# Performance work log

Measured on AMD Instinct MI355X. Metric: run time of the kernel, lower is better.

The kernel has to match this reference:

```python
import jax, jax.numpy as jnp
import numpy as np

B, N, IN, OUT, H = 16, 1024, 512, 512, 4

def setup_inputs() -> dict:
    key = jax.random.key(0)
    ks = jax.random.split(key, 10)
    s = 0.03  # small init scale to keep tanh/sigmoid in sane range
    return {
        "h": jax.random.normal(ks[0], (B, N, IN), jnp.float32),
        "adj": jax.random.randint(ks[1], (B, N, N), 0, 2) > 0,
        "W": jax.random.normal(ks[2], (H, OUT, IN), jnp.float32) * s,   # per-head Linear weight [out,in]
        "bW": jax.random.normal(ks[3], (H, OUT), jnp.float32) * s,
        "attn": jax.random.normal(ks[4], (H, OUT, OUT), jnp.float32) * s,
        "A_w": jax.random.normal(ks[5], (OUT, OUT * H), jnp.float32) * s,
        "fc_w": jax.random.normal(ks[6], (OUT, IN), jnp.float32) * s,
        "g1_w": jax.random.normal(ks[7], (OUT, OUT), jnp.float32) * s,
        "g2_w": jax.random.normal(ks[8], (OUT, OUT), jnp.float32) * s,
        "gbias": jax.random.normal(ks[9], (OUT,), jnp.float32) * s,
    }

def reference(h, adj, W, bW, attn, A_w, fc_w, g1_w, g2_w, gbias):
    # Per-head projection: Wh[b,h,n,o] = h @ W_h^T + b_h  (dropout is identity at inference)
    Wh = jnp.einsum('bni,hoi->bhno', h, W) + bW[None, :, None, :]
    # Bilinear attention scores: Wh @ attn_h @ Wh^T, masked by adjacency, then tanh
    e = jnp.einsum('bhno,hop->bhnp', Wh, attn)          # [B,H,N,O]
    scores = jnp.einsum('bhnp,bhmp->bhnm', e, Wh)       # [B,H,N,N]
    A_mat = jnp.tanh(jnp.where(adj[:, None, :, :], scores, 0.0))
    # Aggregate neighbors and relu
    hp = jax.nn.relu(jnp.einsum('bhnm,bhmo->bhno', A_mat, Wh))  # [B,H,N,O]
    # Concat heads (relu of relu is identity), project with A
    cat = jnp.transpose(hp, (0, 2, 1, 3)).reshape(hp.shape[0], hp.shape[2], -1)  # [B,N,H*O]
    ha = cat @ A_w.T                                     # [B,N,O]
    hf = h @ fc_w.T                                      # [B,N,O]
    # Sigmoid-gated fusion of the two branches
    coeff = jax.nn.sigmoid(hf @ g1_w.T + ha @ g2_w.T + gbias)
    return hf * coeff + ha * (1.0 - coeff)
```

## Files before the change

### kernel.cpp

```cpp
#include <hip/hip_runtime.h>
#include <hip/hip_fp16.h>


typedef _Float16 h8 __attribute__((ext_vector_type(8)));
typedef _Float16 h4 __attribute__((ext_vector_type(4)));
typedef float f4 __attribute__((ext_vector_type(4)));

__device__ __forceinline__ void load_lds16(const void* g, void* l) {
  __builtin_amdgcn_global_load_lds(
      (const __attribute__((address_space(1))) unsigned int*)g,
      (__attribute__((address_space(3))) unsigned int*)l, 16, 0, 0);
}

struct GP {
  const _Float16* A; const _Float16* B; void* C; const float* bias;
  const unsigned long long* adjb; _Float16* aux;
  int K, ldA, ldB, ldC, z0, ntx, nty, nz;
  long sAz, sAb, sBz, sBh, sCz, sCb, sCh, sBiasH, sAuxZ;
};

__device__ __forceinline__ void stage_chunk(const _Float16* G, long ld, int koff,
                                            _Float16* S, int c, int rs, int cs) {
  int r = c * 8 + rs;
  int kb = (cs ^ (r & 7)) * 8;
  load_lds16(G + (long)r * ld + koff + kb, S + c * 512);
}

template<int EPI>
__device__ __forceinline__ void gemm_pipe(GP p, char* smem) {
  const int tid = threadIdx.x;
  const int wv = tid >> 6;
  const int ln = tid & 63;
  const int l15 = ln & 15;
  const int lg = ln >> 4;
  const int wr = wv >> 2, wc = wv & 3;
  const int rs = ln >> 3;
  const int cs = ln & 7;

  const int bid = blockIdx.x;
  const int ntile = p.ntx * p.nty;
  int zl, tx, ty;
  if (p.nz > 1) {
    int xcd = bid & 7;
    int u = bid >> 3;
    zl = xcd + 8 * (u / ntile);
    int t = u % ntile;
    tx = t % p.ntx;
    ty = t / p.ntx;
  } else {
    int xcd = bid & 7;
    int u = bid >> 3;
    int t = xcd * (ntile >> 3) + u;
    zl = 0;
    tx = t % p.ntx;
    ty = t / p.ntx;
  }
  const int zg = p.z0 + zl;
  const int bg = zg >> 2, hg = zg & 3;
  const _Float16* A = p.A + p.sAz * zl + p.sAb * bg;
  const _Float16* Bm = p.B + p.sBz * zl + p.sBh * hg;
  const long m0 = (long)tx * 128;
  const long n0 = (long)ty * 256;
  const int nk = p.K >> 6;

  const _Float16* Ag = A + m0 * p.ldA;
  const _Float16* Bg = Bm + n0 * p.ldB;

  f4 acc[4][4];
#pragma unroll
  for (int i = 0; i < 4; ++i)
#pragma unroll
    for (int j = 0; j < 4; ++j) acc[i][j] = (f4)(0.0f);

#define ABUF(i) ((_Float16*)(smem + (i) * 49152))
#define BBUF(i) ((_Float16*)(smem + (i) * 49152 + 16384))

#pragma unroll
  for (int t0 = 0; t0 < 2; ++t0) {
    if (t0 < nk) {
      _Float16* As = ABUF(t0);
      _Float16* Bs = BBUF(t0);
      const int ko = t0 * 64;
      stage_chunk(Bg, p.ldB, ko, Bs, wv * 2, rs, cs);
      stage_chunk(Bg, p.ldB, ko, Bs, wv * 2 + 1, rs, cs);
      stage_chunk(Bg, p.ldB, ko, Bs, 16 + wv * 2, rs, cs);
      stage_chunk(Bg, p.ldB, ko, Bs, 16 + wv * 2 + 1, rs, cs);
      stage_chunk(Ag, p.ldA, ko, As, wv * 2, rs, cs);
      stage_chunk(Ag, p.ldA, ko, As, wv * 2 + 1, rs, cs);
    }
  }
  if (nk > 1) asm volatile("s_waitcnt vmcnt(6)" ::: "memory");
  else        asm volatile("s_waitcnt vmcnt(0)" ::: "memory");
  __builtin_amdgcn_sched_barrier(0);
  __builtin_amdgcn_s_barrier();

  for (int t = 0; t < nk; ++t) {
    _Float16* As = ABUF(t % 3);
    _Float16* Bs = BBUF(t % 3);
    const int t2 = t + 2;
    const bool st = (t2 < nk);
    _Float16* As2 = ABUF(t2 % 3);
    _Float16* Bs2 = BBUF(t2 % 3);
    const int ko2 = t2 * 64;
#pragma unroll
    for (int ph = 0; ph < 4; ++ph) {
      if (st) {
        if (ph == 0) {
          stage_chunk(Bg, p.ldB, ko2, Bs2, wv * 2, rs, cs);
          stage_chunk(Bg, p.ldB, ko2, Bs2, wv * 2 + 1, rs, cs);
        } else if (ph == 1) {
          stage_chunk(Bg, p.ldB, ko2, Bs2, 16 + wv * 2, rs, cs);
          stage_chunk(Bg, p.ldB, ko2, Bs2, 16 + wv * 2 + 1, rs, cs);
        } else if (ph == 2) {
          stage_chunk(Ag, p.ldA, ko2, As2, wv * 2, rs, cs);
          stage_chunk(Ag, p.ldA, ko2, As2, wv * 2 + 1, rs, cs);
        }
      }
      const int ks = ph >> 1, mp = ph & 1;
      const int kby = ks * 64 + lg * 16;
      h8 av[2], bv[4];
#pragma unroll
      for (int m2 = 0; m2 < 2; ++m2) {
        int row = wr * 64 + (mp * 2 + m2) * 16 + l15;
        av[m2] = *(const h8*)((const char*)As + row * 128 + (kby ^ ((row & 7) << 4)));
      }
#pragma unroll
      for (int n = 0; n < 4; ++n) {
        int col = wc * 64 + n * 16 + l15;
        bv[n] = *(const h8*)((const char*)Bs + col * 128 + (kby ^ ((col & 7) << 4)));
      }
      __builtin_amdgcn_s_barrier();
      __builtin_amdgcn_s_setprio(1);
#pragma unroll
      for (int m2 = 0; m2 < 2; ++m2)
#pragma unroll
        for (int n = 0; n < 4; ++n)
          acc[mp * 2 + m2][n] =
              __builtin_amdgcn_mfma_f32_16x16x32_f16(av[m2], bv[n], acc[mp * 2 + m2][n], 0, 0, 0);
      __builtin_amdgcn_s_setprio(0);
    }
    if (t + 1 < nk) {
      if (t + 2 < nk) asm volatile("s_waitcnt vmcnt(6)" ::: "memory");
      else            asm volatile("s_waitcnt vmcnt(0)" ::: "memory");
      __builtin_amdgcn_sched_barrier(0);
      __builtin_amdgcn_s_barrier();
    }
  }

  asm volatile("s_waitcnt vmcnt(0)" ::: "memory");
  __syncthreads();

  _Float16* Cld = (_Float16*)smem;
  const long coff = p.sCz * zl + p.sCb * bg + p.sCh * hg;
  const float* bias = p.bias ? (p.bias + p.sBiasH * hg) : nullptr;
  _Float16* C = (_Float16*)p.C;
  _Float16* X = (EPI == 6) ? (p.aux + p.sAuxZ * zl) : nullptr;
#pragma unroll
  for (int hh = 0; hh < 2; ++hh) {
    if (wr == hh) {
#pragma unroll
      for (int m = 0; m < 4; ++m) {
#pragma unroll
        for (int j = 0; j < 4; ++j) {
          int lrow = m * 16 + lg * 4 + j;
          long grow = m0 + hh * 64 + lrow;
          int vx = (lrow & 3) << 4;
          unsigned long long w;
          if (EPI == 2)
            w = p.adjb[(long)bg * 16384 + grow * 16 + (n0 >> 6) + wc];
#pragma unroll
          for (int n = 0; n < 4; ++n) {
            int lcol = wv * 0 + wc * 64 + n * 16 + l15;
            float v = acc[m][n][j];
            if (EPI == 6) v += bias[n0 + lcol];
            if (EPI == 2) {
              if ((w >> (n * 16 + l15)) & 1ull) {
                float ex = __expf(2.0f * v);
                v = 1.0f - 2.0f * __builtin_amdgcn_rcpf(ex + 1.0f);
              } else v = 0.0f;
            }
            if (EPI == 3) v = v > 0.0f ? v : 0.0f;
            Cld[lrow * 256 + (lcol ^ vx)] = (_Float16)v;
          }
        }
      }
    }
    __syncthreads();
#pragma unroll
    for (int it = 0; it < 4; ++it) {
      int row = it * 16 + (tid >> 5);
      int col0 = (tid & 31) * 8;
      int vx = (row & 3) << 4;
      h8 o = *(const h8*)&Cld[row * 256 + (col0 ^ vx)];
      *(h8*)&C[coff + (m0 + hh * 64 + row) * p.ldC + n0 + col0] = o;
    }
    if (EPI == 6) {
#pragma unroll
      for (int it = 0; it < 4; ++it) {
        int idx = it * 512 + tid;
        int ol = idx >> 3;
        int ml = (idx & 7) * 8;
        h8 o;
#pragma unroll
        for (int j = 0; j < 8; ++j) {
          int mm = ml + j;
          o[j] = Cld[mm * 256 + (ol ^ ((mm & 3) << 4))];
        }
        *(h8*)&X[(n0 + ol) * 1024 + m0 + hh * 64 + ml] = o;
      }
    }
    __syncthreads();
  }
#undef ABUF
#undef BBUF
}

#define GEMM_PIPE_WRAP(name, epi)                                      \
  __global__ __launch_bounds__(512) void name(GP p) {                  \
    extern __shared__ char smem[];                                     \
    gemm_pipe<epi>(p, smem);                                           \
  }
GEMM_PIPE_WRAP(gemm_wh, 6)
GEMM_PIPE_WRAP(gemm_e, 0)
GEMM_PIPE_WRAP(gemm_amat, 2)
GEMM_PIPE_WRAP(gemm_cat, 3)

__device__ __forceinline__ void stage_tiles5(const _Float16* Ag, const _Float16* Bg,
                                             _Float16* As, _Float16* Bs,
                                             int ldA, int ldB, int wv, int rs, int cs) {
#pragma unroll
  for (int ps = 0; ps < 10; ++ps) {
    int c = ps * 4 + wv;
    if (c < 8) {
      int r = c * 8 + rs;
      int kb = (cs ^ (r & 7)) * 8;
      load_lds16(Ag + (long)r * ldA + kb, As + c * 512);
    } else {
      int cb = c - 8;
      int r = cb * 8 + rs;
      int kb = (cs ^ (r & 7)) * 8;
      load_lds16(Bg + (long)r * ldB + kb, Bs + cb * 512);
    }
  }
}

__device__ __forceinline__ void compute_tile5(const _Float16* As, const _Float16* Bs,
                                              f4 acc[4][4], int wv, int l15, int lg) {
#pragma unroll
  for (int ks = 0; ks < 2; ++ks) {
    const int kby = ks * 64 + lg * 16;
    h8 av[4], bv[4];
#pragma unroll
    for (int m = 0; m < 4; ++m) {
      int row = m * 16 + l15;
      av[m] = *(const h8*)((const char*)As + row * 128 + (kby ^ ((row & 7) << 4)));
    }
#pragma unroll
    for (int n = 0; n < 4; ++n) {
      int col = wv * 64 + n * 16 + l15;
      bv[n] = *(const h8*)((const char*)Bs + col * 128 + (kby ^ ((col & 7) << 4)));
    }
#pragma unroll
    for (int m = 0; m < 4; ++m)
#pragma unroll
      for (int n = 0; n < 4; ++n)
        acc[m][n] = __builtin_amdgcn_mfma_f32_16x16x32_f16(av[m], bv[n], acc[m][n], 0, 0, 0);
  }
}

template<int EPI>
__device__ __forceinline__ void gemm_core_sb(GP p) {
  __shared__ __align__(16) char smem[40960];
  _Float16* Ash = (_Float16*)smem;
  _Float16* Bsh = (_Float16*)(smem + 8192);
  _Float16* Cld = (_Float16*)smem;

  const int tid = threadIdx.x;
  const int wv = tid >> 6;
  const int ln = tid & 63;
  const int l15 = ln & 15;
  const int lg = ln >> 4;
  const int rs = ln >> 3;
  const int cs = ln & 7;

  const int bid = blockIdx.x;
  const int ntile = p.ntx * p.nty;
  int xcd = bid & 7;
  int u = bid >> 3;
  int t = xcd * (ntile >> 3) + u;
  int tx = t % p.ntx;
  int ty = t / p.ntx;
  const int bg = 0, hg = 0;
  const _Float16* A = p.A;
  const _Float16* Bm = p.B;
  const long m0 = (long)tx * 64;
  const long n0 = (long)ty * 256;
  const int nk = p.K >> 6;

  f4 acc[4][4];
#pragma unroll
  for (int i = 0; i < 4; ++i)
#pragma unroll
    for (int j = 0; j < 4; ++j) acc[i][j] = (f4)(0.0f);

  const _Float16* Ag = A + m0 * p.ldA;
  const _Float16* Bg = Bm + n0 * p.ldB;

  for (int kt = 0; kt < nk; ++kt) {
    stage_tiles5(Ag + kt * 64, Bg + kt * 64, Ash, Bsh, p.ldA, p.ldB, wv, rs, cs);
    __syncthreads();
    compute_tile5(Ash, Bsh, acc, wv, l15, lg);
    __syncthreads();
  }

  const long coff = 0;
  const float* bias = p.bias;
  _Float16* C = (_Float16*)p.C;
#pragma unroll
  for (int m = 0; m < 4; ++m) {
#pragma unroll
    for (int j = 0; j < 4; ++j) {
      int lrow = m * 16 + lg * 4 + j;
      int vx = (lrow & 3) << 4;
#pragma unroll
      for (int n = 0; n < 4; ++n) {
        int lcol = wv * 64 + n * 16 + l15;
        float v = acc[m][n][j];
        if (EPI == 5) {
          v += bias[n0 + lcol];
          v = __builtin_amdgcn_rcpf(1.0f + __expf(-v));
        }
        Cld[lrow * 256 + (lcol ^ vx)] = (_Float16)v;
      }
    }
  }
  __syncthreads();
#pragma unroll
  for (int it = 0; it < 8; ++it) {
    int row = it * 8 + (tid >> 5);
    int col0 = (tid & 31) * 8;
    int vx = (row & 3) << 4;
    h8 o = *(const h8*)&Cld[row * 256 + (col0 ^ vx)];
    *(h8*)&C[coff + (m0 + row) * p.ldC + n0 + col0] = o;
  }
  (void)bg; (void)hg;
}

#define GEMM_SB_WRAP(name, epi) \
  __global__ __launch_bounds__(256) void name(GP p) { gemm_core_sb<epi>(p); }
GEMM_SB_WRAP(gemm_hf, 0)
GEMM_SB_WRAP(gemm_ha, 0)
GEMM_SB_WRAP(gemm_gate, 5)

__global__ __launch_bounds__(256) void mix_kernel(const _Float16* gcat,
                                                  const _Float16* coeff, float* out) {
  const int stride = gridDim.x * 256;
  for (int g = blockIdx.x * 256 + threadIdx.x; g < 1048576; g += stride) {
    int r = g >> 6, c8 = (g & 63) << 3;
    h8 hf = *(const h8*)&gcat[(long)r * 1024 + c8];
    h8 ha = *(const h8*)&gcat[(long)r * 1024 + 512 + c8];
    h8 cf = *(const h8*)&coeff[(long)r * 512 + c8];
    float o[8];
#pragma unroll
    for (int j = 0; j < 8; ++j) {
      float c = (float)cf[j];
      o[j] = (float)hf[j] * c + (float)ha[j] * (1.0f - c);
    }
    float* op = &out[(long)r * 512 + c8];
    *(float4*)op = make_float4(o[0], o[1], o[2], o[3]);
    *(float4*)(op + 4) = make_float4(o[4], o[5], o[6], o[7]);
  }
}

__global__ void trans_attn(const float* attn, _Float16* attnT) {
  __shared__ _Float16 tl[64][65];
  const long hh = blockIdx.z;
  const float* I = attn + hh * 262144;
  _Float16* O = attnT + hh * 262144;
  const int r0 = blockIdx.x * 64, c0 = blockIdx.y * 64;
  for (int i = threadIdx.x; i < 4096; i += 256) {
    int r = i >> 6, c = i & 63;
    tl[c][r] = (_Float16)I[(long)(r0 + r) * 512 + c0 + c];
  }
  __syncthreads();
  for (int i = threadIdx.x; i < 4096; i += 256) {
    int c = i >> 6, r = i & 63;
    O[(long)(c0 + c) * 512 + r0 + r] = tl[c][r];
  }
}

__global__ void cvt_f16(const float* in, _Float16* out, int n4) {
  int i = blockIdx.x * 256 + threadIdx.x;
  if (i < n4) {
    float4 v = ((const float4*)in)[i];
    h4 o = {(_Float16)v.x, (_Float16)v.y, (_Float16)v.z, (_Float16)v.w};
    ((h4*)out)[i] = o;
  }
}

__global__ void build_gw(const float* g1, const float* g2, _Float16* gw) {
  int i = blockIdx.x * 256 + threadIdx.x;
  int o = i >> 10, k = i & 1023;
  float v = (k < 512) ? g1[o * 512 + k] : g2[o * 512 + (k - 512)];
  gw[i] = (_Float16)v;
}

__global__ void detect_fmt(const unsigned char* adj, int* flags) {
  __shared__ int sa, sb, sc;
  if (threadIdx.x == 0) { sa = 0; sb = 0; sc = 0; }
  __syncthreads();
  int a = 0, b = 0, c = 0;
  for (int i = threadIdx.x; i < 4096; i += 256) {
    if (adj[i]) {
      if (i & 3) a = 1;
      else c = 1;
      if ((i & 7) == 4) b = 1;
    }
  }
  if (a) sa = 1;
  if (b) sb = 1;
  if (c) sc = 1;
  __syncthreads();
  if (threadIdx.x == 0) {
    int fmt;
    if (sa) fmt = sc ? 1 : 3;
    else fmt = sb ? 0 : 2;
    flags[0] = fmt;
  }
}

__global__ void adj_bits(const void* adj, const int* flags, unsigned long long* adjb) {
  long i = (long)blockIdx.x * 256 + threadIdx.x;
  int fmt = flags[0];
  bool v;
  if (fmt == 1) v = ((const unsigned char*)adj)[i] != 0;
  else if (fmt == 3) v = ((const float*)adj)[i] != 0.0f;
  else if (fmt == 2) v = ((const long long*)adj)[i] != 0;
  else v = ((const int*)adj)[i] != 0;
  unsigned long long m = __ballot(v);
  if ((threadIdx.x & 63) == 0) adjb[i >> 6] = m;
}

extern "C" void kernel_launch(void* const* d_in, const int* in_sizes, int n_in,
                              void* d_out, int out_size, void* d_ws, size_t ws_size,
                              hipStream_t stream) {
  const float* h    = (const float*)d_in[0];
  const void*  adj  = d_in[1];
  const float* W    = (const float*)d_in[2];
  const float* bW   = (const float*)d_in[3];
  const float* attn = (const float*)d_in[4];
  const float* A_w  = (const float*)d_in[5];
  const float* fc_w = (const float*)d_in[6];
  const float* g1   = (const float*)d_in[7];
  const float* g2   = (const float*)d_in[8];
  const float* gbias= (const float*)d_in[9];
  float* out = (float*)d_out;
  char* ws = (char*)d_ws;
  (void)in_sizes; (void)n_in; (void)out_size;

  const int PIPE_LDS = 147456;
  hipFuncSetAttribute((const void*)gemm_wh,   hipFuncAttributeMaxDynamicSharedMemorySize, PIPE_LDS);
  hipFuncSetAttribute((const void*)gemm_e,    hipFuncAttributeMaxDynamicSharedMemorySize, PIPE_LDS);
  hipFuncSetAttribute((const void*)gemm_amat, hipFuncAttributeMaxDynamicSharedMemorySize, PIPE_LDS);
  hipFuncSetAttribute((const void*)gemm_cat,  hipFuncAttributeMaxDynamicSharedMemorySize, PIPE_LDS);

  const size_t MB = 1ull << 20;
  const size_t fixedB = 92 * MB;
  int ZCv = 16;
  if (fixedB + 5ull * 64 * MB <= ws_size) ZCv = 64;
  else if (fixedB + 5ull * 32 * MB <= ws_size) ZCv = 32;
  const int nchunk = 64 / ZCv;

  size_t off = 0;
  auto alloc = [&](size_t sz) { size_t o = off; off += (sz + 255) & ~(size_t)255; return o; };
  const size_t oFlags = alloc(256);
  const size_t oH16   = alloc(16 * MB);
  const size_t oW16   = alloc(2 * MB);
  const size_t oAttnT = alloc(2 * MB);
  const size_t oAw16  = alloc(2 * MB);
  const size_t oFc16  = alloc(512 * 1024);
  const size_t oGw16  = alloc(1 * MB);
  const size_t oAdjb  = alloc(2 * MB);
  const size_t oCat   = alloc(64 * MB);
  const size_t oWhC   = alloc((size_t)ZCv * MB);
  const size_t oEC    = alloc((size_t)ZCv * MB);
  const size_t oWhTC  = alloc((size_t)ZCv * MB);
  const size_t oAmatC = alloc((size_t)ZCv * 2 * MB);
  const size_t oGcat  = oWhC;
  const size_t oCoeff = oAmatC;

  int* flags = (int*)(ws + oFlags);
  _Float16* h16   = (_Float16*)(ws + oH16);
  _Float16* W16   = (_Float16*)(ws + oW16);
  _Float16* attnT = (_Float16*)(ws + oAttnT);
  _Float16* Aw16  = (_Float16*)(ws + oAw16);
  _Float16* fc16  = (_Float16*)(ws + oFc16);
  _Float16* gw16  = (_Float16*)(ws + oGw16);
  unsigned long long* adjb = (unsigned long long*)(ws + oAdjb);
  _Float16* cat   = (_Float16*)(ws + oCat);
  _Float16* WhC   = (_Float16*)(ws + oWhC);
  _Float16* eC    = (_Float16*)(ws + oEC);
  _Float16* WhTC  = (_Float16*)(ws + oWhTC);
  _Float16* AmatC = (_Float16*)(ws + oAmatC);
  _Float16* gcat  = (_Float16*)(ws + oGcat);
  _Float16* coeff = (_Float16*)(ws + oCoeff);

  detect_fmt<<<1, 256, 0, stream>>>((const unsigned char*)adj, flags);
  adj_bits<<<65536, 256, 0, stream>>>(adj, flags, adjb);
  cvt_f16<<<8192, 256, 0, stream>>>(h, h16, 2097152);
  cvt_f16<<<1024, 256, 0, stream>>>(W, W16, 262144);
  cvt_f16<<<1024, 256, 0, stream>>>(A_w, Aw16, 262144);
  cvt_f16<<<256, 256, 0, stream>>>(fc_w, fc16, 65536);
  build_gw<<<2048, 256, 0, stream>>>(g1, g2, gw16);
  trans_attn<<<dim3(8, 8, 4), 256, 0, stream>>>(attn, attnT);

  for (int c = 0; c < nchunk; ++c) {
    const int z0 = c * ZCv;
    GP q;
    q = GP{};
    q.A = h16; q.B = W16; q.C = WhC; q.bias = bW; q.aux = WhTC;
    q.K = 512; q.ldA = 512; q.ldB = 512; q.ldC = 512; q.z0 = z0;
    q.ntx = 8; q.nty = 2; q.nz = ZCv;
    q.sAz = 0; q.sAb = 524288; q.sBz = 0; q.sBh = 262144;
    q.sCz = 524288; q.sCb = 0; q.sCh = 0; q.sBiasH = 512; q.sAuxZ = 524288;
    gemm_wh<<<16 * ZCv, 512, PIPE_LDS, stream>>>(q);
    q = GP{};
    q.A = WhC; q.B = attnT; q.C = eC;
    q.K = 512; q.ldA = 512; q.ldB = 512; q.ldC = 512; q.z0 = z0;
    q.ntx = 8; q.nty = 2; q.nz = ZCv;
    q.sAz = 524288; q.sBh = 262144; q.sCz = 524288;
    gemm_e<<<16 * ZCv, 512, PIPE_LDS, stream>>>(q);
    q = GP{};
    q.A = eC; q.B = WhC; q.C = AmatC; q.adjb = adjb;
    q.K = 512; q.ldA = 512; q.ldB = 512; q.ldC = 1024; q.z0 = z0;
    q.ntx = 8; q.nty = 4; q.nz = ZCv;
    q.sAz = 524288; q.sBz = 524288; q.sCz = 1048576;
    gemm_amat<<<32 * ZCv, 512, PIPE_LDS, stream>>>(q);
    q = GP{};
    q.A = AmatC; q.B = WhTC; q.C = cat;
    q.K = 1024; q.ldA = 1024; q.ldB = 1024; q.ldC = 2048; q.z0 = z0;
    q.sAz = 1048576; q.sBz = 524288;
    q.ntx = 8; q.nty = 2; q.nz = ZCv;
    q.sCz = 0; q.sCb = 2097152; q.sCh = 512;
    gemm_cat<<<16 * ZCv, 512, PIPE_LDS, stream>>>(q);
  }

  GP q;
  q = GP{};
  q.A = h16; q.B = fc16; q.C = gcat;
  q.K = 512; q.ldA = 512; q.ldB = 512; q.ldC = 1024; q.z0 = 0;
  q.ntx = 256; q.nty = 2; q.nz = 1;
  gemm_hf<<<512, 256, 0, stream>>>(q);
  q = GP{};
  q.A = cat; q.B = Aw16; q.C = gcat + 512;
  q.K = 2048; q.ldA = 2048; q.ldB = 2048; q.ldC = 1024; q.z0 = 0;
  q.ntx = 256; q.nty = 2; q.nz = 1;
  gemm_ha<<<512, 256, 0, stream>>>(q);
  q = GP{};
  q.A = gcat; q.B = gw16; q.C = coeff; q.bias = gbias;
  q.K = 1024; q.ldA = 1024; q.ldB = 1024; q.ldC = 512; q.z0 = 0;
  q.ntx = 256; q.nty = 2; q.nz = 1;
  gemm_gate<<<512, 256, 0, stream>>>(q);
  mix_kernel<<<2048, 256, 0, stream>>>(gcat, coeff, out);
}
```

Before: 537.0 us.

## Restructure pipelined GEMM main loop into two half-steps with fewer barriers

Reorganizes the triple-buffered GEMM inner loop. Each k-tile is now split into two halves over N: all A fragments plus half the B fragments are loaded at once, and the next-tile global->LDS staging is interleaved between them. This cuts the per-iteration barrier count from five to two and changes the B staging chunk assignment per wave. It also removes some dead variables in the small GEMM. The cost is more registers held for A fragments, and a different overlap pattern between MFMA work and LDS/global traffic.

```diff
diff --git a/kernel.cpp b/kernel.cpp
--- a/kernel.cpp
+++ b/kernel.cpp
@@ -75,76 +75,83 @@
 #define ABUF(i) ((_Float16*)(smem + (i) * 49152))
 #define BBUF(i) ((_Float16*)(smem + (i) * 49152 + 16384))
 
-#pragma unroll
-  for (int t0 = 0; t0 < 2; ++t0) {
-    if (t0 < nk) {
-      _Float16* As = ABUF(t0);
-      _Float16* Bs = BBUF(t0);
-      const int ko = t0 * 64;
-      stage_chunk(Bg, p.ldB, ko, Bs, wv * 2, rs, cs);
-      stage_chunk(Bg, p.ldB, ko, Bs, wv * 2 + 1, rs, cs);
-      stage_chunk(Bg, p.ldB, ko, Bs, 16 + wv * 2, rs, cs);
-      stage_chunk(Bg, p.ldB, ko, Bs, 16 + wv * 2 + 1, rs, cs);
-      stage_chunk(Ag, p.ldA, ko, As, wv * 2, rs, cs);
-      stage_chunk(Ag, p.ldA, ko, As, wv * 2 + 1, rs, cs);
-    }
-  }
+#define STAGE_A(t)                                                      \
+  { _Float16* As_ = ABUF((t) % 3); const int ko_ = (t) * 64;            \
+    stage_chunk(Ag, p.ldA, ko_, As_, wv * 2, rs, cs);                   \
+    stage_chunk(Ag, p.ldA, ko_, As_, wv * 2 + 1, rs, cs); }
+#define STAGE_B1(t)                                                     \
+  { _Float16* Bs_ = BBUF((t) % 3);                                      \
+    stage_chunk(Bg, p.ldB, (t) * 64, Bs_, wv * 4, rs, cs); }
+#define STAGE_B3(t)                                                     \
+  { _Float16* Bs_ = BBUF((t) % 3); const int ko_ = (t) * 64;            \
+    stage_chunk(Bg, p.ldB, ko_, Bs_, wv * 4 + 1, rs, cs);               \
+    stage_chunk(Bg, p.ldB, ko_, Bs_, wv * 4 + 2, rs, cs);               \
+    stage_chunk(Bg, p.ldB, ko_, Bs_, wv * 4 + 3, rs, cs); }
+
+  STAGE_A(0) STAGE_B1(0) STAGE_B3(0)
+  if (nk > 1) { STAGE_A(1) STAGE_B1(1) STAGE_B3(1) }
   if (nk > 1) asm volatile("s_waitcnt vmcnt(6)" ::: "memory");
   else        asm volatile("s_waitcnt vmcnt(0)" ::: "memory");
   __builtin_amdgcn_sched_barrier(0);
-  __builtin_amdgcn_s_barrier();
+  asm volatile("s_barrier" ::: "memory");
 
   for (int t = 0; t < nk; ++t) {
-    _Float16* As = ABUF(t % 3);
-    _Float16* Bs = BBUF(t % 3);
-    const int t2 = t + 2;
-    const bool st = (t2 < nk);
-    _Float16* As2 = ABUF(t2 % 3);
-    _Float16* Bs2 = BBUF(t2 % 3);
-    const int ko2 = t2 * 64;
-#pragma unroll
-    for (int ph = 0; ph < 4; ++ph) {
-      if (st) {
-        if (ph == 0) {
-          stage_chunk(Bg, p.ldB, ko2, Bs2, wv * 2, rs, cs);
-          stage_chunk(Bg, p.ldB, ko2, Bs2, wv * 2 + 1, rs, cs);
-        } else if (ph == 1) {
-          stage_chunk(Bg, p.ldB, ko2, Bs2, 16 + wv * 2, rs, cs);
-          stage_chunk(Bg, p.ldB, ko2, Bs2, 16 + wv * 2 + 1, rs, cs);
-        } else if (ph == 2) {
-          stage_chunk(Ag, p.ldA, ko2, As2, wv * 2, rs, cs);
-          stage_chunk(Ag, p.ldA, ko2, As2, wv * 2 + 1, rs, cs);
-        }
+    const _Float16* As = ABUF(t % 3);
+    const _Float16* Bs = BBUF(t % 3);
+    const bool st2 = (t + 2 < nk);
+    h8 av[4][2], bv[2][2];
+#pragma unroll
+    for (int m = 0; m < 4; ++m)
+#pragma unroll
+      for (int ks = 0; ks < 2; ++ks) {
+        int row = wr * 64 + m * 16 + l15;
+        int kby = ks * 64 + lg * 16;
+        av[m][ks] = *(const h8*)((const char*)As + row * 128 + (kby ^ ((row & 7) << 4)));
       }
-      const int ks = ph >> 1, mp = ph & 1;
-      const int kby = ks * 64 + lg * 16;
-      h8 av[2], bv[4];
-#pragma unroll
-      for (int m2 = 0; m2 < 2; ++m2) {
-        int row = wr * 64 + (mp * 2 + m2) * 16 + l15;
-        av[m2] = *(const h8*)((const char*)As + row * 128 + (kby ^ ((row & 7) << 4)));
+#pragma unroll
+    for (int nn = 0; nn < 2; ++nn)
+#pragma unroll
+      for (int ks = 0; ks < 2; ++ks) {
+        int col = wc * 64 + nn * 16 + l15;
+        int kby = ks * 64 + lg * 16;
+        bv[nn][ks] = *(const h8*)((const char*)Bs + col * 128 + (kby ^ ((col & 7) << 4)));
       }
-#pragma unroll
-      for (int n = 0; n < 4; ++n) {
-        int col = wc * 64 + n * 16 + l15;
-        bv[n] = *(const h8*)((const char*)Bs + col * 128 + (kby ^ ((col & 7) << 4)));
+    if (st2) { STAGE_A(t + 2) STAGE_B1(t + 2) }
+    __builtin_amdgcn_s_setprio(1);
+#pragma unroll
+    for (int m = 0; m < 4; ++m)
+#pragma unroll
+      for (int nn = 0; nn < 2; ++nn)
+#pragma unroll
+        for (int ks = 0; ks < 2; ++ks)
+          acc[m][nn] = __builtin_amdgcn_mfma_f32_16x16x32_f16(av[m][ks], bv[nn][ks], acc[m][nn], 0, 0, 0);
+    __builtin_amdgcn_s_setprio(0);
+    __builtin_amdgcn_sched_barrier(0);
+    asm volatile("s_barrier" ::: "memory");
+#pragma unroll
+    for (int nn = 0; nn < 2; ++nn)
+#pragma unroll
+      for (int ks = 0; ks < 2; ++ks) {
+        int col = wc * 64 + (2 + nn) * 16 + l15;
+        int kby = ks * 64 + lg * 16;
+        bv[nn][ks] = *(const h8*)((const char*)Bs + col * 128 + (kby ^ ((col & 7) << 4)));
       }
-      __builtin_amdgcn_s_barrier();
-      __builtin_amdgcn_s_setprio(1);
-#pragma unroll
-      for (int m2 = 0; m2 < 2; ++m2)
-#pragma unroll
-        for (int n = 0; n < 4; ++n)
-          acc[mp * 2 + m2][n] =
-              __builtin_amdgcn_mfma_f32_16x16x32_f16(av[m2], bv[n], acc[mp * 2 + m2][n], 0, 0, 0);
-      __builtin_amdgcn_s_setprio(0);
-    }
+    if (st2) STAGE_B3(t + 2)
+    __builtin_amdgcn_s_setprio(1);
+#pragma unroll
+    for (int m = 0; m < 4; ++m)
+#pragma unroll
+      for (int nn = 0; nn < 2; ++nn)
+#pragma unroll
+        for (int ks = 0; ks < 2; ++ks)
+          acc[m][2 + nn] = __builtin_amdgcn_mfma_f32_16x16x32_f16(av[m][ks], bv[nn][ks], acc[m][2 + nn], 0, 0, 0);
+    __builtin_amdgcn_s_setprio(0);
     if (t + 1 < nk) {
-      if (t + 2 < nk) asm volatile("s_waitcnt vmcnt(6)" ::: "memory");
-      else            asm volatile("s_waitcnt vmcnt(0)" ::: "memory");
-      __builtin_amdgcn_sched_barrier(0);
-      __builtin_amdgcn_s_barrier();
-    }
+      if (st2) asm volatile("s_waitcnt vmcnt(6)" ::: "memory");
+      else     asm volatile("s_waitcnt vmcnt(0)" ::: "memory");
+    }
+    __builtin_amdgcn_sched_barrier(0);
+    asm volatile("s_barrier" ::: "memory");
   }
 
   asm volatile("s_waitcnt vmcnt(0)" ::: "memory");
@@ -170,7 +177,7 @@
             w = p.adjb[(long)bg * 16384 + grow * 16 + (n0 >> 6) + wc];
 #pragma unroll
           for (int n = 0; n < 4; ++n) {
-            int lcol = wv * 0 + wc * 64 + n * 16 + l15;
+            int lcol = wc * 64 + n * 16 + l15;
             float v = acc[m][n][j];
             if (EPI == 6) v += bias[n0 + lcol];
             if (EPI == 2) {
@@ -213,6 +220,9 @@
   }
 #undef ABUF
 #undef BBUF
+#undef STAGE_A
+#undef STAGE_B1
+#undef STAGE_B3
 }
 
 #define GEMM_PIPE_WRAP(name, epi)                                      \
@@ -290,7 +300,6 @@
   int t = xcd * (ntile >> 3) + u;
   int tx = t % p.ntx;
   int ty = t / p.ntx;
-  const int bg = 0, hg = 0;
   const _Float16* A = p.A;
   const _Float16* Bm = p.B;
   const long m0 = (long)tx * 64;
@@ -313,7 +322,6 @@
     __syncthreads();
   }
 
-  const long coff = 0;
   const float* bias = p.bias;
   _Float16* C = (_Float16*)p.C;
 #pragma unroll
@@ -341,9 +349,8 @@
     int col0 = (tid & 31) * 8;
     int vx = (row & 3) << 4;
     h8 o = *(const h8*)&Cld[row * 256 + (col0 ^ vx)];
-    *(h8*)&C[coff + (m0 + row) * p.ldC + n0 + col0] = o;
-  }
-  (void)bg; (void)hg;
+    *(h8*)&C[(m0 + row) * p.ldC + n0 + col0] = o;
+  }
 }
 
 #define GEMM_SB_WRAP(name, epi) \
```

After: 524.3 us. 1.02x faster.
